# Optimization experiments

Hardware: AMD Instinct MI355X
Metric: run time of the kernel (lower is better)

Reference implementation:

```python
import jax, jax.numpy as jnp
import numpy as np

DIM = 512
K_ALL = 11
K_TOP = 4
DOMAIN = 10
EPS = 1e-12
NEG_INF = -1e30

def _normalize(x):
    n = jnp.linalg.norm(x, axis=-1, keepdims=True)
    return x / jnp.maximum(n, EPS)

def _leaky(x):
    return jax.nn.leaky_relu(x, 0.01)

def setup_inputs():
    key = jax.random.key(0)
    ks = jax.random.split(key, 16)
    Bp, Lp, Bg, Lg = 128, 256, 64, 512
    probes = jax.random.normal(ks[0], (1, Bp, Lp, DIM), jnp.float32)
    gallery = jax.random.normal(ks[1], (1, Bg, Lg, DIM), jnp.float32)
    probe_lengths = jax.random.randint(ks[2], (1, Bp), 1, Lp + 1)
    gallery_lengths = jax.random.randint(ks[3], (1, Bg), 1, Lg + 1)
    proxies_p = jax.random.normal(ks[4], (K_ALL, DIM), jnp.float32) * 0.06
    proxies_g = jax.random.normal(ks[5], (K_ALL, DIM), jnp.float32) * 0.06
    transform_W = jax.random.normal(ks[6], (DOMAIN, DIM), jnp.float32) * 0.06
    transform_b = jnp.zeros((DOMAIN,), jnp.float32)
    probe_W = jnp.eye(DIM, dtype=jnp.float32)  # nn.init.eye_
    probe_b = jnp.zeros((DIM,), jnp.float32)
    # pooler MLP weights stacked over the 11 experts; init_weights: N(0, 0.001), zero bias
    pool_W1 = jax.random.normal(ks[7], (K_ALL, 2 * DIM, 3 * DIM), jnp.float32) * 1e-3
    pool_b1 = jnp.zeros((K_ALL, 2 * DIM), jnp.float32)
    pool_W2 = jax.random.normal(ks[8], (K_ALL, 2 * DIM, 2 * DIM), jnp.float32) * 1e-3
    pool_b2 = jnp.zeros((K_ALL, 2 * DIM), jnp.float32)
    pool_W3 = jax.random.normal(ks[9], (K_ALL, DIM, 2 * DIM), jnp.float32) * 1e-3
    pool_b3 = jnp.zeros((K_ALL, DIM), jnp.float32)
    return dict(probes=probes, gallery=gallery, probe_lengths=probe_lengths,
                gallery_lengths=gallery_lengths, proxies_p=proxies_p, proxies_g=proxies_g,
                transform_W=transform_W, transform_b=transform_b, probe_W=probe_W,
                probe_b=probe_b, pool_W1=pool_W1, pool_b1=pool_b1, pool_W2=pool_W2,
                pool_b2=pool_b2, pool_W3=pool_W3, pool_b3=pool_b3)

def reference(probes, gallery, probe_lengths, gallery_lengths, proxies_p, proxies_g,
              transform_W, transform_b, probe_W, probe_b,
              pool_W1, pool_b1, pool_W2, pool_b2, pool_W3, pool_b3):
    def fuse(feat, length, proxies, use_probe_linear):
        # feat: [L, D], length: scalar int; masked equivalent of feat[:length]
        L = feat.shape[0]
        fmask = (jnp.arange(L) < length).astype(feat.dtype)[:, None]  # [L, 1]
        lp = jnp.maximum(length, 1).astype(feat.dtype)
        normed = _normalize(feat)
        tf = _normalize(feat @ transform_W.T + transform_b)        # [L, 10]
        tp = _normalize(proxies @ transform_W.T + transform_b)      # [K_ALL, 10]
        sims = tf @ tp.T                                            # [L, K_ALL]
        gsim = (sims * fmask).sum(0)                                # [K_ALL]
        _, idx = jax.lax.top_k(gsim, K_TOP)
        mean = (feat * fmask).sum(0) / lp                           # [D]
        var = (((feat - mean) ** 2) * fmask).sum(0) / lp            # biased variance
        summary = jnp.concatenate([jnp.tile(mean[None], (K_TOP, 1)),
                                   jnp.tile(var[None], (K_TOP, 1)),
                                   proxies[idx]], axis=-1)          # [K_TOP, 3D]
        # expert-gathered pooler MLPs (dropout = identity in eval)
        h = _leaky(jnp.einsum('koi,ki->ko', pool_W1[idx], summary) + pool_b1[idx])
        h = _leaky(jnp.einsum('koi,ki->ko', pool_W2[idx], h) + pool_b2[idx])
        ctx = _leaky(jnp.einsum('koi,ki->ko', pool_W3[idx], h) + pool_b3[idx])  # [K_TOP, D]
        q = feat @ probe_W.T + probe_b if use_probe_linear else feat
        scores = q @ ctx.T                                          # [L, K_TOP]
        scores = jnp.where(fmask > 0, scores, NEG_INF)
        w = jax.nn.softmax(scores, axis=0)                          # softmax over set dim
        return jnp.einsum('ld,lk->kd', normed, w)                   # [K_TOP, D]

    p, g = probes[0], gallery[0]
    pl, gl = probe_lengths[0], gallery_lengths[0]
    final_probe = jax.vmap(lambda f, l: fuse(f, l, proxies_p, True))(p, pl)
    final_gallery = jax.vmap(lambda f, l: fuse(f, l, proxies_g, False))(g, gl)
    return (final_probe,
            proxies_p @ transform_W.T + transform_b,
            final_gallery,
            proxies_g @ transform_W.T + transform_b)
```

## Files before the change

### kernel.cpp

```cpp
#include <hip/hip_runtime.h>
#include <hip/hip_bf16.h>

namespace {

using us = unsigned short;
typedef __attribute__((ext_vector_type(8))) short bf16x8;
typedef __attribute__((ext_vector_type(4))) float f32x4;
typedef __attribute__((ext_vector_type(4))) unsigned short us4;
typedef __attribute__((ext_vector_type(4))) unsigned int u32x4;

constexpr int DIM_ = 512, KALL = 11, DOM = 10, NPROBE = 128, NSETS = 192;
constexpr int LPR = 256, LGA = 512;

constexpr size_t O_OUT1 = 0;
constexpr size_t O_OUT2 = (size_t)NPROBE * 4 * DIM_;
constexpr size_t O_OUT3 = O_OUT2 + KALL * DOM;
constexpr size_t O_OUT4 = O_OUT3 + (size_t)64 * 4 * DIM_;

constexpr size_t F_TP   = 64;
constexpr size_t F_IDX  = 320;
constexpr size_t F_S0A  = 1600;
constexpr size_t F_WQ   = 4096;
constexpr size_t F_GP   = 495616;
constexpr size_t F_SUMM = 514048;
constexpr size_t F_H1   = 612352;
constexpr size_t F_PART = F_H1;
constexpr size_t F_CTXW = F_H1;
constexpr size_t F_H2   = 1693696;
constexpr size_t F_ACC  = F_H2;
constexpr size_t F_CTX  = 2775040;
constexpr size_t F_WT   = 3315712;
constexpr size_t WS_FLOATS = 3446784;
constexpr size_t WS_BYTES  = WS_FLOATS * 4;

__device__ __forceinline__ float b2f(us u) { return __uint_as_float(((unsigned)u) << 16); }
__device__ __forceinline__ us f2b(float x) {
    unsigned u = __float_as_uint(x);
    u += 0x7FFF + ((u >> 16) & 1);
    return (us)(u >> 16);
}
__device__ __forceinline__ float ldT(const float* p) { return *p; }
__device__ __forceinline__ float ldT(const us* p) { return b2f(*p); }
__device__ __forceinline__ void stT(float* p, float v) { *p = v; }
__device__ __forceinline__ void stT(us* p, float v) { *p = f2b(v); }

__device__ __forceinline__ bf16x8 loadA(const us* p) { return *(const bf16x8*)p; }
__device__ __forceinline__ bf16x8 loadA(const float* p) {
    f32x4 a = *(const f32x4*)p, b = *(const f32x4*)(p + 4);
    bf16x8 r;
#pragma unroll
    for (int j = 0; j < 4; ++j) { r[j] = (short)f2b(a[j]); r[4 + j] = (short)f2b(b[j]); }
    return r;
}

__device__ __forceinline__ void gload_lds16(const us* g, us* l) {
    __builtin_amdgcn_global_load_lds(
        (const __attribute__((address_space(1))) void*)g,
        (__attribute__((address_space(3))) void*)l, 16, 0, 0);
}

__device__ __forceinline__ void decode64(int bx, int& set, int& base, int& L) {
    if (bx < 512) { set = bx >> 2; base = (bx & 3) * 64; L = LPR; }
    else { set = NPROBE + ((bx - 512) >> 3); base = ((bx - 512) & 7) * 64; L = LGA; }
}

__global__ void detect_kernel(const unsigned int* probeW_bits, int* flag) {
    if (threadIdx.x == 0) *flag = (probeW_bits[0] == 0x3F800000u) ? 0 : 1;
}

template <typename T>
__device__ void proxies_body(const T* pp, const T* pg, const T* tW, const T* tb,
                             float* wsf, T* dout) {
    int b = blockIdx.x;
    int fam = b / KALL, i = b % KALL;
    int lane = threadIdx.x;
    const T* src = fam ? pg : pp;
    float t[DOM];
#pragma unroll
    for (int r = 0; r < DOM; ++r) t[r] = 0.f;
    for (int d = lane; d < DIM_; d += 64) {
        float x = ldT(src + (size_t)i * DIM_ + d);
#pragma unroll
        for (int r = 0; r < DOM; ++r) t[r] += x * ldT(tW + (size_t)r * DIM_ + d);
    }
#pragma unroll
    for (int off = 32; off >= 1; off >>= 1)
#pragma unroll
        for (int r = 0; r < DOM; ++r) t[r] += __shfl_xor(t[r], off, 64);
#pragma unroll
    for (int r = 0; r < DOM; ++r) t[r] += ldT(tb + r);
    float nn = 0.f;
#pragma unroll
    for (int r = 0; r < DOM; ++r) nn += t[r] * t[r];
    float inv = 1.0f / fmaxf(sqrtf(nn), 1e-12f);
    if (lane < DOM) {
        size_t base = fam ? O_OUT4 : O_OUT2;
        stT(dout + base + i * DOM + lane, t[lane]);
        wsf[F_TP + fam * 128 + i * DOM + lane] = t[lane] * inv;
    }
}
__global__ void proxies_kernel(const int* flag, const void* pp, const void* pg,
                               const void* tW, const void* tb, float* wsf, void* dout) {
    if (*flag)
        proxies_body<us>((const us*)pp, (const us*)pg, (const us*)tW, (const us*)tb, wsf, (us*)dout);
    else
        proxies_body<float>((const float*)pp, (const float*)pg, (const float*)tW, (const float*)tb, wsf, (float*)dout);
}

template <typename T>
__device__ void sums_body(const T* probes, const T* gallery, const int* plen,
                          const int* glen, float* wsf) {
    int bx = blockIdx.x, set = bx >> 2, c = bx & 3;
    bool probe = set < NPROBE;
    int L = probe ? LPR : LGA;
    const T* feat = probe ? probes + (size_t)set * L * DIM_
                          : gallery + (size_t)(set - NPROBE) * L * DIM_;
    int len = probe ? plen[set] : glen[set - NPROBE];
    int len_eff = min(max(len, 1), L);
    int r0 = (c * len_eff) >> 2, r1 = ((c + 1) * len_eff) >> 2;
    __shared__ float psum[DIM_], psq[DIM_];
    int tid = threadIdx.x, w = tid >> 6, lane = tid & 63;
    psum[tid] = 0.f; psum[tid + 256] = 0.f;
    psq[tid] = 0.f; psq[tid + 256] = 0.f;
    __syncthreads();
    float asum[8] = {0,0,0,0,0,0,0,0}, asq[8] = {0,0,0,0,0,0,0,0};
    for (int l = r0 + w * 2; l < r1; l += 8) {
        bool two = (l + 1 < r1);
        float f0[8], f1[8];
        if constexpr (sizeof(T) == 2) {
            u32x4 ra = *(const u32x4*)(feat + (size_t)l * DIM_ + lane * 8);
            u32x4 rb = two ? *(const u32x4*)(feat + (size_t)(l + 1) * DIM_ + lane * 8)
                           : (u32x4){0, 0, 0, 0};
#pragma unroll
            for (int q = 0; q < 4; ++q) {
                f0[2*q] = __uint_as_float(ra[q] << 16);
                f0[2*q+1] = __uint_as_float(ra[q] & 0xFFFF0000u);
                f1[2*q] = __uint_as_float(rb[q] << 16);
                f1[2*q+1] = __uint_as_float(rb[q] & 0xFFFF0000u);
            }
        } else {
            const T* rp = feat + (size_t)l * DIM_ + lane * 8;
            f32x4 a0 = *(const f32x4*)rp, a1 = *(const f32x4*)(rp + 4);
#pragma unroll
            for (int j = 0; j < 4; ++j) { f0[j] = a0[j]; f0[4+j] = a1[j]; }
            if (two) {
                const T* rq = feat + (size_t)(l + 1) * DIM_ + lane * 8;
                f32x4 b0 = *(const f32x4*)rq, b1 = *(const f32x4*)(rq + 4);
#pragma unroll
                for (int j = 0; j < 4; ++j) { f1[j] = b0[j]; f1[4+j] = b1[j]; }
            } else {
#pragma unroll
                for (int j = 0; j < 8; ++j) f1[j] = 0.f;
            }
        }
#pragma unroll
        for (int j = 0; j < 8; ++j) {
            asum[j] += f0[j] + f1[j];
            asq[j] += f0[j] * f0[j] + f1[j] * f1[j];
        }
    }
#pragma unroll
    for (int j = 0; j < 8; ++j) {
        atomicAdd(&psum[lane * 8 + j], asum[j]);
        atomicAdd(&psq[lane * 8 + j], asq[j]);
    }
    __syncthreads();
    float* P = wsf + F_PART + (size_t)bx * 1024;
    P[tid] = psum[tid]; P[tid + 256] = psum[tid + 256];
    P[512 + tid] = psq[tid]; P[768 + tid] = psq[tid + 256];
}
__global__ __launch_bounds__(256) void sums_kernel(const int* flag, const void* probes,
        const void* gallery, const int* plen, const int* glen, float* wsf) {
    if (*flag) sums_body<us>((const us*)probes, (const us*)gallery, plen, glen, wsf);
    else sums_body<float>((const float*)probes, (const float*)gallery, plen, glen, wsf);
}

template <typename T>
__device__ void sims_body(const T* probes, const T* gallery, const int* plen,
                          const int* glen, const T* tW, float* wsf) {
    int bx = blockIdx.x, set, base, L;
    decode64(bx, set, base, L);
    bool probe = set < NPROBE;
    int len = probe ? plen[set] : glen[set - NPROBE];
    int len_eff = min(max(len, 1), L);
    float* GP = wsf + F_GP + (size_t)bx * 12;
    int tid = threadIdx.x;
    if (base >= len_eff) { if (tid < KALL) GP[tid] = 0.f; return; }
    const T* feat = probe ? probes + (size_t)set * L * DIM_
                          : gallery + (size_t)(set - NPROBE) * L * DIM_;
    __shared__ __align__(16) float tile[4][320];
    __shared__ float tpl[KALL * DOM];
    __shared__ float gs[16];
    if (tid < KALL * DOM) tpl[tid] = wsf[F_TP + (probe ? 0 : 128) + tid];
    if (tid < 16) gs[tid] = 0.f;
    int w = tid >> 6, lane = tid & 63, lm = lane & 15, quad = lane >> 4;

    bf16x8 bq[16];
#pragma unroll
    for (int s = 0; s < 16; ++s) {
        if (lm < DOM) bq[s] = loadA(tW + (size_t)lm * DIM_ + s * 32 + quad * 8);
        else bq[s] = (bf16x8){0, 0, 0, 0, 0, 0, 0, 0};
    }
    int m0 = base + w * 16;
    const T* Ap = feat + (size_t)(m0 + lm) * DIM_ + quad * 8;
    f32x4 acc = (f32x4){0.f, 0.f, 0.f, 0.f};
    float vsq = 0.f;
#pragma unroll
    for (int s = 0; s < 16; ++s) {
        bf16x8 a;
        if constexpr (sizeof(T) == 2) {
            a = *(const bf16x8*)(Ap + s * 32);
#pragma unroll
            for (int j = 0; j < 8; ++j) { float x = b2f((us)a[j]); vsq += x * x; }
        } else {
            f32x4 p0 = *(const f32x4*)(Ap + s * 32), p1 = *(const f32x4*)(Ap + s * 32 + 4);
#pragma unroll
            for (int j = 0; j < 4; ++j) {
                vsq += p0[j] * p0[j] + p1[j] * p1[j];
                a[j] = (short)f2b(p0[j]); a[4 + j] = (short)f2b(p1[j]);
            }
        }
        acc = __builtin_amdgcn_mfma_f32_16x16x32_bf16(a, bq[s], acc, 0, 0, 0);
    }
    vsq += __shfl_xor(vsq, 16, 64);
    vsq += __shfl_xor(vsq, 32, 64);
    {
        int rown = m0 + lm;
        if (quad == 0 && rown < len_eff)
            wsf[F_WQ + (size_t)set * 2560 + (size_t)rown * 5 + 4] =
                1.0f / fmaxf(sqrtf(vsq), 1e-12f);
    }
#pragma unroll
    for (int r = 0; r < 4; ++r) tile[w][(quad * 4 + r) * 20 + lm] = acc[r];
    __syncthreads();

    float gacc[KALL];
#pragma unroll
    for (int k = 0; k < KALL; ++k) gacc[k] = 0.f;
    if (lane < 16) {
        int row = m0 + lane;
        if (row < len_eff) {
            const float* tr = &tile[w][lane * 20];
            f32x4 t0 = *(const f32x4*)tr, t1 = *(const f32x4*)(tr + 4);
            float tv[DOM] = {t0[0], t0[1], t0[2], t0[3], t1[0], t1[1], t1[2], t1[3], tr[8], tr[9]};
            float nn = 0.f;
#pragma unroll
            for (int r = 0; r < DOM; ++r) nn += tv[r] * tv[r];
            float inv = 1.0f / fmaxf(sqrtf(nn), 1e-12f);
#pragma unroll
            for (int k = 0; k < KALL; ++k) {
                float s = 0.f;
#pragma unroll
                for (int r = 0; r < DOM; ++r) s += tv[r] * tpl[k * DOM + r];
                gacc[k] = s * inv;
            }
        }
    }
#pragma unroll
    for (int off = 8; off >= 1; off >>= 1)
#pragma unroll
        for (int k = 0; k < KALL; ++k) gacc[k] += __shfl_xor(gacc[k], off, 64);
    if (lane == 0)
#pragma unroll
        for (int k = 0; k < KALL; ++k) atomicAdd(&gs[k], gacc[k]);
    __syncthreads();
    if (tid < KALL) GP[tid] = gs[tid];
}
__global__ __launch_bounds__(256, 3) void sims_kernel(const int* flag, const void* probes,
        const void* gallery, const int* plen, const int* glen, const void* tW, float* wsf) {
    if (*flag) sims_body<us>((const us*)probes, (const us*)gallery, plen, glen, (const us*)tW, wsf);
    else sims_body<float>((const float*)probes, (const float*)gallery, plen, glen, (const float*)tW, wsf);
}

__global__ void statsfin_kernel(const int* plen, const int* glen, float* wsf) {
    int set = blockIdx.x, tid = threadIdx.x;
    bool probe = set < NPROBE;
    int len = probe ? plen[set] : glen[set - NPROBE];
    float lp = (float)max(len, 1);
    const float* P = wsf + F_PART + (size_t)set * 4 * 1024;
    us* SUMM = (us*)(wsf + F_SUMM);
    for (int d = tid; d < DIM_; d += 256) {
        float s = P[d] + P[1024 + d] + P[2048 + d] + P[3072 + d];
        float q = P[512 + d] + P[1536 + d] + P[2560 + d] + P[3584 + d];
        float m = s / lp;
        float v = q / lp - m * m;
        SUMM[(size_t)set * 1024 + d] = f2b(m);
        SUMM[(size_t)set * 1024 + DIM_ + d] = f2b(v);
    }
    if (tid == 0) {
        int nch = probe ? 4 : 8;
        int gb = probe ? set * 4 : 512 + (set - NPROBE) * 8;
        float g[KALL];
        for (int i = 0; i < KALL; ++i) {
            float s = 0.f;
            for (int c = 0; c < nch; ++c) s += wsf[F_GP + (size_t)(gb + c) * 12 + i];
            g[i] = s;
        }
        int* idx4 = (int*)(wsf + F_IDX);
        for (int kk = 0; kk < 4; ++kk) {
            int bi = 0; float bv = g[0];
            for (int i = 1; i < KALL; ++i)
                if (g[i] > bv) { bv = g[i]; bi = i; }
            idx4[set * 4 + kk] = bi;
            g[bi] = -3e38f;
        }
    }
}

template <typename T>
__device__ void wt_body(const T* W, us* WT) {
    __shared__ us t[64][65];
    int bi = blockIdx.y * 64, bj = blockIdx.x * 64, tid = threadIdx.x;
    for (int i = tid; i < 4096; i += 256) {
        int r = i >> 6, cc = i & 63;
        t[r][cc] = (sizeof(T) == 2) ? ((const us*)W)[(size_t)(bi + r) * DIM_ + bj + cc]
                                    : f2b(ldT(W + (size_t)(bi + r) * DIM_ + bj + cc));
    }
    __syncthreads();
    for (int i = tid; i < 4096; i += 256) {
        int r = i >> 6, cc = i & 63;
        WT[(size_t)(bj + r) * DIM_ + bi + cc] = t[cc][r];
    }
}
__global__ void wt_kernel(const int* flag, const void* W, us* WT) {
    if (*flag) wt_body<us>((const us*)W, WT);
    else wt_body<float>((const float*)W, WT);
}

template <int M, int KTOT, int L1>
__global__ __launch_bounds__(256) void mlp_one(const int* flag, const void* Wv,
        const void* biasv, const void* ppv, const void* pgv, const us* X, us* Y) {
    constexpr int MT = M / 64;
    int flagv = *flag;
    __shared__ us SM[16384];
    us* As = SM;
    us* Bs = SM + 8192;
    int bx = blockIdx.x;
    int nt = bx / (MT * KALL);
    int rem = bx - nt * (MT * KALL);
    int e = rem % KALL;
    int mt = rem / KALL;
    int tid = threadIdx.x, w = tid >> 6, lane = tid & 63;
    int lm = lane & 15, quad = lane >> 4;
    const int RS = L1 ? 1024 : KTOT;
    int s0 = nt * 64;
    int srow = tid >> 4;
    int csrc = (tid & 15) ^ (srow & 7);
    us* lA = As + tid * 8;
    us* lB = Bs + tid * 8;
    const size_t arow = (size_t)e * M + mt * 64 + srow;
    const us*    AbB = (const us*)Wv + arow * KTOT + csrc * 8;
    const float* AbF = (const float*)Wv + arow * KTOT + csrc * 8;
    const us* Xbase = X + ((size_t)(L1 ? 0 : e * NSETS) + s0 + srow) * RS + csrc * 8;
    const us* PbB = nullptr;
    const float* PbF = nullptr;
    if (L1) {
        PbB = (const us*)(nt < 2 ? ppv : pgv) + (size_t)e * DIM_ + csrc * 8;
        PbF = (const float*)(nt < 2 ? ppv : pgv) + (size_t)e * DIM_ + csrc * 8;
    }
    f32x4 acc[4];
#pragma unroll
    for (int j = 0; j < 4; ++j) acc[j] = (f32x4){0.f, 0.f, 0.f, 0.f};
    int ar = w * 16 + lm, aswz = ar & 7;

    for (int k0 = 0; k0 < KTOT; k0 += 128) {
        __syncthreads();
        if (flagv) {
#pragma unroll
            for (int i = 0; i < 4; ++i)
                gload_lds16(AbB + (size_t)(i * 16) * KTOT + k0, lA + i * 2048);
        } else {
#pragma unroll
            for (int i = 0; i < 4; ++i)
                *(bf16x8*)(lA + i * 2048) = loadA(AbF + (size_t)(i * 16) * KTOT + k0);
        }
        if (!L1 || k0 < 1024) {
#pragma unroll
            for (int i = 0; i < 4; ++i)
                gload_lds16(Xbase + (size_t)(i * 16) * RS + k0, lB + i * 2048);
        } else if (flagv) {
#pragma unroll
            for (int i = 0; i < 4; ++i)
                gload_lds16(PbB + (k0 - 1024), lB + i * 2048);
        } else {
            bf16x8 v = loadA(PbF + (k0 - 1024));
#pragma unroll
            for (int i = 0; i < 4; ++i)
                *(bf16x8*)(lB + i * 2048) = v;
        }
        __syncthreads();
#pragma unroll
        for (int ks = 0; ks < 4; ++ks) {
            int cg = ks * 4 + quad;
            bf16x8 a = *(const bf16x8*)(As + ar * 128 + ((cg ^ aswz) * 8));
#pragma unroll
            for (int j = 0; j < 4; ++j) {
                int br = j * 16 + lm;
                bf16x8 b = *(const bf16x8*)(Bs + br * 128 + ((cg ^ (br & 7)) * 8));
                acc[j] = __builtin_amdgcn_mfma_f32_16x16x32_bf16(a, b, acc[j], 0, 0, 0);
            }
        }
    }
    int m0 = mt * 64 + w * 16 + quad * 4;
    float bv[4];
#pragma unroll
    for (int r = 0; r < 4; ++r)
        bv[r] = flagv ? b2f(((const us*)biasv)[(size_t)e * M + m0 + r])
                      : ((const float*)biasv)[(size_t)e * M + m0 + r];
#pragma unroll
    for (int j = 0; j < 4; ++j) {
        int s = s0 + j * 16 + lm;
        us4 pk;
#pragma unroll
        for (int r = 0; r < 4; ++r) {
            float v = acc[j][r] + bv[r];
            v = v > 0.f ? v : 0.01f * v;
            pk[r] = f2b(v);
        }
        *(us4*)(Y + ((size_t)e * NSETS + s) * M + m0) = pk;
    }
}

__global__ void fold_kernel(const us* CTX, const us* WT, us* CTXW) {
    int nt = blockIdx.x, mtb = blockIdx.y;
    int e = mtb >> 1, sub = mtb & 1;
    int row0 = e * NSETS + sub * 64;
    int tid = threadIdx.x, w = tid >> 6, lane = tid & 63;
    int lm = lane & 15, quad = lane >> 4, kq = quad * 8;
    const us* Ap = CTX + ((size_t)row0 + w * 16 + lm) * DIM_ + kq;
    int n0 = nt * 64;
    const us* Bp = WT + (size_t)(n0 + lm) * DIM_ + kq;
    f32x4 acc[4];
#pragma unroll
    for (int j = 0; j < 4; ++j) acc[j] = (f32x4){0.f, 0.f, 0.f, 0.f};
#pragma unroll 2
    for (int kc = 0; kc < DIM_; kc += 32) {
        bf16x8 a = *(const bf16x8*)(Ap + kc);
#pragma unroll
        for (int j = 0; j < 4; ++j) {
            bf16x8 b = *(const bf16x8*)(Bp + kc + (size_t)j * 16 * DIM_);
            acc[j] = __builtin_amdgcn_mfma_f32_16x16x32_bf16(a, b, acc[j], 0, 0, 0);
        }
    }
    int mrow = row0 + w * 16 + quad * 4;
#pragma unroll
    for (int j = 0; j < 4; ++j)
#pragma unroll
        for (int r = 0; r < 4; ++r)
            CTXW[(size_t)(mrow + r) * DIM_ + n0 + j * 16 + lm] = f2b(acc[j][r]);
}

template <typename T>
__device__ void s0a_body(const us* CTX, const T* pb, float* S0A) {
    int tid = threadIdx.x, w = tid >> 6, lane = tid & 63;
    int row = blockIdx.x * 4 + w;
    bf16x8 cv = *(const bf16x8*)(CTX + (size_t)row * DIM_ + lane * 8);
    float s = 0.f;
#pragma unroll
    for (int j = 0; j < 8; ++j) s += b2f((us)cv[j]) * ldT(pb + lane * 8 + j);
#pragma unroll
    for (int off = 32; off >= 1; off >>= 1) s += __shfl_xor(s, off, 64);
    if (lane == 0) S0A[row] = s;
}
__global__ void s0a_kernel(const int* flag, const us* CTX, const void* pb, float* S0A) {
    if (*flag) s0a_body<us>(CTX, (const us*)pb, S0A);
    else s0a_body<float>(CTX, (const float*)pb, S0A);
}

template <typename T>
__device__ void score_body(const T* probes, const T* gallery, const int* plen,
                           const int* glen, float* wsf) {
    int bx = blockIdx.x, set, base, L;
    decode64(bx, set, base, L);
    bool probe = set < NPROBE;
    int len = probe ? plen[set] : glen[set - NPROBE];
    int len_eff = min(max(len, 1), L);
    if (base >= len_eff) return;
    const T* feat = probe ? probes + (size_t)set * L * DIM_
                          : gallery + (size_t)(set - NPROBE) * L * DIM_;
    int tid = threadIdx.x, w = tid >> 6, lane = tid & 63;
    int lm = lane & 15, quad = lane >> 4;
    const int* idx4 = (const int*)(wsf + F_IDX);
    const us* CTXW = (const us*)(wsf + F_CTXW);
    const us* CTXR = (const us*)(wsf + F_CTX);
    bf16x8 bq[16];
    float s0v = 0.f;
    if (lm < 4) {
        int row = idx4[set * 4 + lm] * NSETS + set;
        const us* src = (probe ? CTXW : CTXR) + (size_t)row * DIM_ + quad * 8;
#pragma unroll
        for (int s = 0; s < 16; ++s) bq[s] = *(const bf16x8*)(src + s * 32);
        s0v = probe ? wsf[F_S0A + row] : 0.f;
    } else {
#pragma unroll
        for (int s = 0; s < 16; ++s) bq[s] = (bf16x8){0, 0, 0, 0, 0, 0, 0, 0};
    }
    int m0 = base + w * 16;
    const T* Ap = feat + (size_t)(m0 + lm) * DIM_ + quad * 8;
    f32x4 acc = (f32x4){0.f, 0.f, 0.f, 0.f};
#pragma unroll
    for (int s = 0; s < 16; ++s) {
        bf16x8 a = loadA(Ap + s * 32);
        acc = __builtin_amdgcn_mfma_f32_16x16x32_bf16(a, bq[s], acc, 0, 0, 0);
    }
    if (lm < 4) {
        float* wq = wsf + F_WQ + (size_t)set * 2560;
#pragma unroll
        for (int r = 0; r < 4; ++r) {
            int row = m0 + quad * 4 + r;
            wq[(size_t)row * 5 + lm] = acc[r] + s0v;
        }
    }
}
__global__ __launch_bounds__(256, 3) void score_kernel(const int* flag, const void* probes,
        const void* gallery, const int* plen, const int* glen, float* wsf) {
    if (*flag) score_body<us>((const us*)probes, (const us*)gallery, plen, glen, wsf);
    else score_body<float>((const float*)probes, (const float*)gallery, plen, glen, wsf);
}

__global__ void softmax_kernel(const int* plen, const int* glen, float* wsf) {
    int set = blockIdx.x, tid = threadIdx.x, k = tid >> 6, lane = tid & 63;
    bool probe = set < NPROBE;
    int L = probe ? LPR : LGA;
    int len = probe ? plen[set] : glen[set - NPROBE];
    int len_eff = min(max(len, 1), L);
    float* wq = wsf + F_WQ + (size_t)set * 2560;
    float cv[8];
    int n = 0;
    float m = -3e38f;
    for (int l = lane; l < len_eff; l += 64) {
        cv[n] = wq[(size_t)l * 5 + k];
        m = fmaxf(m, cv[n]);
        ++n;
    }
#pragma unroll
    for (int off = 32; off >= 1; off >>= 1) m = fmaxf(m, __shfl_xor(m, off, 64));
    float se = 0.f;
    for (int i = 0; i < n; ++i) se += __expf(cv[i] - m);
#pragma unroll
    for (int off = 32; off >= 1; off >>= 1) se += __shfl_xor(se, off, 64);
    float invs = 1.0f / se;
    n = 0;
    for (int l = lane; l < len_eff; l += 64) {
        wq[(size_t)l * 5 + k] = __expf(cv[n] - m) * invs * wq[(size_t)l * 5 + 4];
        ++n;
    }
}

template <typename T>
__device__ void accum_body(const T* probes, const T* gallery, const int* plen,
                           const int* glen, float* wsf) {
    int bx = blockIdx.x, set = bx >> 2, c = bx & 3;
    bool probe = set < NPROBE;
    int L = probe ? LPR : LGA;
    const T* feat = probe ? probes + (size_t)set * L * DIM_
                          : gallery + (size_t)(set - NPROBE) * L * DIM_;
    int len = probe ? plen[set] : glen[set - NPROBE];
    int len_eff = min(max(len, 1), L);
    int r0 = (c * len_eff) >> 2, r1 = ((c + 1) * len_eff) >> 2;
    int tid = threadIdx.x, g = tid >> 8, t = tid & 255;
    __shared__ float cf[512];
    __shared__ float pbuf[2048];
    int nr = r1 - r0;
    const float* wq = wsf + F_WQ + (size_t)set * 2560;
    for (int p = tid; p < nr * 4; p += 512)
        cf[p] = wq[(size_t)(r0 + (p >> 2)) * 5 + (p & 3)];
    __syncthreads();
    float ac[8] = {0.f, 0.f, 0.f, 0.f, 0.f, 0.f, 0.f, 0.f};
#pragma unroll 4
    for (int l = r0 + g; l < r1; l += 2) {
        float f0, f1;
        if constexpr (sizeof(T) == 2) {
            unsigned u = *(const unsigned*)((const us*)feat + (size_t)l * DIM_ + t * 2);
            f0 = __uint_as_float(u << 16);
            f1 = __uint_as_float(u & 0xFFFF0000u);
        } else {
            const T* rp = feat + (size_t)l * DIM_ + t * 2;
            f0 = rp[0]; f1 = rp[1];
        }
        f32x4 cc = *(const f32x4*)&cf[(l - r0) * 4];
#pragma unroll
        for (int k = 0; k < 4; ++k) {
            ac[k * 2] += f0 * cc[k];
            ac[k * 2 + 1] += f1 * cc[k];
        }
    }
    if (g == 1) {
#pragma unroll
        for (int i = 0; i < 8; ++i) pbuf[i * 256 + t] = ac[i];
    }
    __syncthreads();
    if (g == 0) {
        float* P = wsf + F_ACC + (size_t)bx * 2048;
#pragma unroll
        for (int k = 0; k < 4; ++k) {
            P[k * 512 + t * 2] = ac[k * 2] + pbuf[(k * 2) * 256 + t];
            P[k * 512 + t * 2 + 1] = ac[k * 2 + 1] + pbuf[(k * 2 + 1) * 256 + t];
        }
    }
}
__global__ __launch_bounds__(512) void accum_kernel(const int* flag, const void* probes,
        const void* gallery, const int* plen, const int* glen, float* wsf) {
    if (*flag) accum_body<us>((const us*)probes, (const us*)gallery, plen, glen, wsf);
    else accum_body<float>((const float*)probes, (const float*)gallery, plen, glen, wsf);
}

template <typename T>
__device__ void reduce_body(const float* wsf, T* dout) {
    int set = blockIdx.x, d = threadIdx.x;
    const float* A = wsf + F_ACC + (size_t)set * 4 * 2048;
    size_t ob = (set < NPROBE) ? O_OUT1 + (size_t)set * 2048
                               : O_OUT3 + (size_t)(set - NPROBE) * 2048;
#pragma unroll
    for (int k = 0; k < 4; ++k) {
        float s = A[k * 512 + d] + A[2048 + k * 512 + d] + A[4096 + k * 512 + d] + A[6144 + k * 512 + d];
        stT(dout + ob + k * 512 + d, s);
    }
}
__global__ __launch_bounds__(512) void reduce_kernel(const int* flag, const float* wsf, void* dout) {
    if (*flag) reduce_body<us>(wsf, (us*)dout);
    else reduce_body<float>(wsf, (float*)dout);
}

}

extern "C" void kernel_launch(void* const* d_in, const int* in_sizes, int n_in,
                              void* d_out, int out_size, void* d_ws, size_t ws_size,
                              hipStream_t stream) {
    if (ws_size < WS_BYTES) return;
    float* wsf = (float*)d_ws;
    int* flag = (int*)d_ws;
    us* SUMM = (us*)(wsf + F_SUMM);
    us* H1 = (us*)(wsf + F_H1);
    us* H2 = (us*)(wsf + F_H2);
    us* CTXb = (us*)(wsf + F_CTX);
    us* CTXW = (us*)(wsf + F_CTXW);
    us* WT = (us*)(wsf + F_WT);
    const int* plen = (const int*)d_in[2];
    const int* glen = (const int*)d_in[3];

    detect_kernel<<<1, 64, 0, stream>>>((const unsigned int*)d_in[8], flag);
    proxies_kernel<<<22, 64, 0, stream>>>(flag, d_in[4], d_in[5], d_in[6], d_in[7], wsf, d_out);
    wt_kernel<<<dim3(8, 8), 256, 0, stream>>>(flag, d_in[8], WT);
    sums_kernel<<<NSETS * 4, 256, 0, stream>>>(flag, d_in[0], d_in[1], plen, glen, wsf);
    sims_kernel<<<1024, 256, 0, stream>>>(flag, d_in[0], d_in[1], plen, glen, d_in[6], wsf);
    statsfin_kernel<<<NSETS, 256, 0, stream>>>(plen, glen, wsf);

    mlp_one<1024, 1536, 1><<<3 * 16 * KALL, 256, 0, stream>>>(
        flag, d_in[10], d_in[11], d_in[4], d_in[5], SUMM, H1);
    mlp_one<1024, 1024, 0><<<3 * 16 * KALL, 256, 0, stream>>>(
        flag, d_in[12], d_in[13], d_in[4], d_in[5], H1, H2);
    mlp_one<512, 1024, 0><<<3 * 8 * KALL, 256, 0, stream>>>(
        flag, d_in[14], d_in[15], d_in[4], d_in[5], H2, CTXb);

    fold_kernel<<<dim3(8, 22), 256, 0, stream>>>(CTXb, WT, CTXW);
    s0a_kernel<<<528, 256, 0, stream>>>(flag, CTXb, d_in[9], wsf + F_S0A);
    score_kernel<<<1024, 256, 0, stream>>>(flag, d_in[0], d_in[1], plen, glen, wsf);
    softmax_kernel<<<NSETS, 256, 0, stream>>>(plen, glen, wsf);
    accum_kernel<<<NSETS * 4, 512, 0, stream>>>(flag, d_in[0], d_in[1], plen, glen, wsf);
    reduce_kernel<<<NSETS, 512, 0, stream>>>(flag, wsf, d_out);
}
```

Baseline: 415.6 us.

## Fold proxy term of first MLP layer into bias and double-buffer MLP GEMM

The constant proxy slice of the first pooler layer (the last 512 input columns) is now precomputed once per expert as an effective bias for the probe side and the gallery side, in a new small kernel. This shrinks the layer-1 GEMM reduction from 1536 to 1024. The MLP GEMM kernel is also restructured: weight fragments are loaded straight into registers instead of through LDS, and activation tiles use a double-buffered LDS pipeline with 64-wide K steps, so loads overlap compute. The cost is one extra launch and a fixed 16-step K loop, which assumes every layer's K is 1024.

Result: slower. 429.5 us (+3.4%).

```diff
diff --git a/kernel.cpp b/kernel.cpp
--- a/kernel.cpp
+++ b/kernel.cpp
@@ -30,7 +30,8 @@
 constexpr size_t F_ACC  = F_H2;
 constexpr size_t F_CTX  = 2775040;
 constexpr size_t F_WT   = 3315712;
-constexpr size_t WS_FLOATS = 3446784;
+constexpr size_t F_BEFF = 3446784;
+constexpr size_t WS_FLOATS = F_BEFF + 2 * KALL * 1024;
 constexpr size_t WS_BYTES  = WS_FLOATS * 4;
 
 __device__ __forceinline__ float b2f(us u) { return __uint_as_float(((unsigned)u) << 16); }
@@ -47,6 +48,12 @@
 __device__ __forceinline__ bf16x8 loadA(const us* p) { return *(const bf16x8*)p; }
 __device__ __forceinline__ bf16x8 loadA(const float* p) {
     f32x4 a = *(const f32x4*)p, b = *(const f32x4*)(p + 4);
+    bf16x8 r;
+#pragma unroll
+    for (int j = 0; j < 4; ++j) { r[j] = (short)f2b(a[j]); r[4 + j] = (short)f2b(b[j]); }
+    return r;
+}
+__device__ __forceinline__ bf16x8 pack8(f32x4 a, f32x4 b) {
     bf16x8 r;
 #pragma unroll
     for (int j = 0; j < 4; ++j) { r[j] = (short)f2b(a[j]); r[4 + j] = (short)f2b(b[j]); }
@@ -105,6 +112,55 @@
         proxies_body<us>((const us*)pp, (const us*)pg, (const us*)tW, (const us*)tb, wsf, (us*)dout);
     else
         proxies_body<float>((const float*)pp, (const float*)pg, (const float*)tW, (const float*)tb, wsf, (float*)dout);
+}
+
+template <typename T>
+__device__ void pbias_body(const T* W1, const T* b1, const T* pp, const T* pg, float* beff) {
+    int bx = blockIdx.x;
+    int e = bx >> 4, ch = bx & 15;
+    int tid = threadIdx.x;
+    int om = tid >> 2, sub = tid & 3;
+    int m = ch * 64 + om;
+    const T* wr = W1 + ((size_t)e * 1024 + m) * 1536 + 1024 + sub * 128;
+    const T* pr = pp + (size_t)e * DIM_ + sub * 128;
+    const T* gr = pg + (size_t)e * DIM_ + sub * 128;
+    float sp = 0.f, sg = 0.f;
+    if constexpr (sizeof(T) == 2) {
+#pragma unroll 4
+        for (int k = 0; k < 128; k += 2) {
+            unsigned wv = *(const unsigned*)(wr + k);
+            unsigned pv = *(const unsigned*)(pr + k);
+            unsigned gv = *(const unsigned*)(gr + k);
+            float w0 = __uint_as_float(wv << 16), w1 = __uint_as_float(wv & 0xFFFF0000u);
+            float p0 = __uint_as_float(pv << 16), p1 = __uint_as_float(pv & 0xFFFF0000u);
+            float g0 = __uint_as_float(gv << 16), g1 = __uint_as_float(gv & 0xFFFF0000u);
+            sp += w0 * p0 + w1 * p1;
+            sg += w0 * g0 + w1 * g1;
+        }
+    } else {
+#pragma unroll 2
+        for (int k = 0; k < 128; k += 4) {
+            f32x4 wv = *(const f32x4*)(wr + k);
+            f32x4 pv = *(const f32x4*)(pr + k);
+            f32x4 gv = *(const f32x4*)(gr + k);
+#pragma unroll
+            for (int q = 0; q < 4; ++q) { sp += wv[q] * pv[q]; sg += wv[q] * gv[q]; }
+        }
+    }
+    sp += __shfl_xor(sp, 1, 64); sp += __shfl_xor(sp, 2, 64);
+    sg += __shfl_xor(sg, 1, 64); sg += __shfl_xor(sg, 2, 64);
+    if (sub == 0) {
+        float bb = ldT(b1 + (size_t)e * 1024 + m);
+        beff[(size_t)e * 1024 + m] = bb + sp;
+        beff[(size_t)(KALL + e) * 1024 + m] = bb + sg;
+    }
+}
+__global__ void pbias_kernel(const int* flag, const void* W1, const void* b1,
+                             const void* pp, const void* pg, float* beff) {
+    if (*flag)
+        pbias_body<us>((const us*)W1, (const us*)b1, (const us*)pp, (const us*)pg, beff);
+    else
+        pbias_body<float>((const float*)W1, (const float*)b1, (const float*)pp, (const float*)pg, beff);
 }
 
 template <typename T>
@@ -327,14 +383,13 @@
     else wt_body<float>((const float*)W, WT);
 }
 
-template <int M, int KTOT, int L1>
+template <int M, int KS, int L1>
 __global__ __launch_bounds__(256) void mlp_one(const int* flag, const void* Wv,
-        const void* biasv, const void* ppv, const void* pgv, const us* X, us* Y) {
+        const void* biasv, const us* X, us* Y, const float* beff) {
     constexpr int MT = M / 64;
+    constexpr int NK = 16;
     int flagv = *flag;
-    __shared__ us SM[16384];
-    us* As = SM;
-    us* Bs = SM + 8192;
+    __shared__ us SM[8192];
     int bx = blockIdx.x;
     int nt = bx / (MT * KALL);
     int rem = bx - nt * (MT * KALL);
@@ -342,71 +397,91 @@
     int mt = rem / KALL;
     int tid = threadIdx.x, w = tid >> 6, lane = tid & 63;
     int lm = lane & 15, quad = lane >> 4;
-    const int RS = L1 ? 1024 : KTOT;
     int s0 = nt * 64;
-    int srow = tid >> 4;
-    int csrc = (tid & 15) ^ (srow & 7);
-    us* lA = As + tid * 8;
-    us* lB = Bs + tid * 8;
-    const size_t arow = (size_t)e * M + mt * 64 + srow;
-    const us*    AbB = (const us*)Wv + arow * KTOT + csrc * 8;
-    const float* AbF = (const float*)Wv + arow * KTOT + csrc * 8;
-    const us* Xbase = X + ((size_t)(L1 ? 0 : e * NSETS) + s0 + srow) * RS + csrc * 8;
-    const us* PbB = nullptr;
-    const float* PbF = nullptr;
-    if (L1) {
-        PbB = (const us*)(nt < 2 ? ppv : pgv) + (size_t)e * DIM_ + csrc * 8;
-        PbF = (const float*)(nt < 2 ? ppv : pgv) + (size_t)e * DIM_ + csrc * 8;
-    }
+    const size_t aoff = ((size_t)e * M + mt * 64 + w * 16 + lm) * KS + quad * 8;
+    const float* AF = (const float*)Wv + aoff;
+    const us*    AB = (const us*)Wv + aoff;
+    int xrow0 = (L1 ? 0 : e * NSETS) + s0;
+    int slot0 = w * 64 + lane, slot1 = slot0 + 256;
+    int brow0 = slot0 >> 3, bcol0 = (slot0 & 7) ^ (brow0 & 7);
+    int brow1 = slot1 >> 3, bcol1 = (slot1 & 7) ^ (brow1 & 7);
+    const us* Xs0 = X + ((size_t)(xrow0 + brow0)) * 1024 + bcol0 * 8;
+    const us* Xs1 = X + ((size_t)(xrow0 + brow1)) * 1024 + bcol1 * 8;
+    us* ls0 = SM + slot0 * 8;
+    us* ls1 = SM + slot1 * 8;
+
     f32x4 acc[4];
 #pragma unroll
     for (int j = 0; j < 4; ++j) acc[j] = (f32x4){0.f, 0.f, 0.f, 0.f};
-    int ar = w * 16 + lm, aswz = ar & 7;
-
-    for (int k0 = 0; k0 < KTOT; k0 += 128) {
-        __syncthreads();
+
+    bf16x8 a0[2], a1[2];
+    f32x4 pan[4];
+
+    auto issueB = [&](int par, int k0) {
+        gload_lds16(Xs0 + k0, ls0 + par * 4096);
+        gload_lds16(Xs1 + k0, ls1 + par * 4096);
+    };
+    auto loadAx = [&](int k0, bf16x8* adst) {
         if (flagv) {
-#pragma unroll
-            for (int i = 0; i < 4; ++i)
-                gload_lds16(AbB + (size_t)(i * 16) * KTOT + k0, lA + i * 2048);
+            adst[0] = *(const bf16x8*)(AB + k0);
+            adst[1] = *(const bf16x8*)(AB + k0 + 32);
         } else {
-#pragma unroll
-            for (int i = 0; i < 4; ++i)
-                *(bf16x8*)(lA + i * 2048) = loadA(AbF + (size_t)(i * 16) * KTOT + k0);
-        }
-        if (!L1 || k0 < 1024) {
-#pragma unroll
-            for (int i = 0; i < 4; ++i)
-                gload_lds16(Xbase + (size_t)(i * 16) * RS + k0, lB + i * 2048);
-        } else if (flagv) {
-#pragma unroll
-            for (int i = 0; i < 4; ++i)
-                gload_lds16(PbB + (k0 - 1024), lB + i * 2048);
-        } else {
-            bf16x8 v = loadA(PbF + (k0 - 1024));
-#pragma unroll
-            for (int i = 0; i < 4; ++i)
-                *(bf16x8*)(lB + i * 2048) = v;
-        }
-        __syncthreads();
-#pragma unroll
-        for (int ks = 0; ks < 4; ++ks) {
-            int cg = ks * 4 + quad;
-            bf16x8 a = *(const bf16x8*)(As + ar * 128 + ((cg ^ aswz) * 8));
+            pan[0] = *(const f32x4*)(AF + k0);
+            pan[1] = *(const f32x4*)(AF + k0 + 4);
+            pan[2] = *(const f32x4*)(AF + k0 + 32);
+            pan[3] = *(const f32x4*)(AF + k0 + 36);
+        }
+    };
+    auto packA = [&](bf16x8* adst) {
+        if (!flagv) {
+            adst[0] = pack8(pan[0], pan[1]);
+            adst[1] = pack8(pan[2], pan[3]);
+        }
+    };
+    auto compute = [&](int par, const bf16x8* a) {
+        const us* Bb = SM + par * 4096;
+#pragma unroll
+        for (int ks = 0; ks < 2; ++ks)
 #pragma unroll
             for (int j = 0; j < 4; ++j) {
                 int br = j * 16 + lm;
-                bf16x8 b = *(const bf16x8*)(Bs + br * 128 + ((cg ^ (br & 7)) * 8));
-                acc[j] = __builtin_amdgcn_mfma_f32_16x16x32_bf16(a, b, acc[j], 0, 0, 0);
+                int cg = ks * 4 + quad;
+                bf16x8 b = *(const bf16x8*)(Bb + br * 64 + ((cg ^ (br & 7)) * 8));
+                acc[j] = __builtin_amdgcn_mfma_f32_16x16x32_bf16(a[ks], b, acc[j], 0, 0, 0);
             }
-        }
-    }
+    };
+
+    issueB(0, 0);
+    loadAx(0, a0);
+    packA(a0);
+    __syncthreads();
+#pragma unroll 1
+    for (int t = 0; t < NK; t += 2) {
+        int k1 = (t + 1) * 64, k2 = (t + 2) * 64;
+        if (t + 1 < NK) { issueB(1, k1); loadAx(k1, a1); }
+        compute(0, a0);
+        if (t + 1 < NK) packA(a1);
+        __syncthreads();
+        if (t + 1 < NK) {
+            if (t + 2 < NK) { issueB(0, k2); loadAx(k2, a0); }
+            compute(1, a1);
+            if (t + 2 < NK) packA(a0);
+            __syncthreads();
+        }
+    }
+
     int m0 = mt * 64 + w * 16 + quad * 4;
     float bv[4];
-#pragma unroll
-    for (int r = 0; r < 4; ++r)
-        bv[r] = flagv ? b2f(((const us*)biasv)[(size_t)e * M + m0 + r])
-                      : ((const float*)biasv)[(size_t)e * M + m0 + r];
+    if (L1) {
+        const float* be = beff + ((size_t)((nt < 2) ? 0 : KALL) + e) * 1024 + m0;
+#pragma unroll
+        for (int r = 0; r < 4; ++r) bv[r] = be[r];
+    } else {
+#pragma unroll
+        for (int r = 0; r < 4; ++r)
+            bv[r] = flagv ? b2f(((const us*)biasv)[(size_t)e * M + m0 + r])
+                          : ((const float*)biasv)[(size_t)e * M + m0 + r];
+    }
 #pragma unroll
     for (int j = 0; j < 4; ++j) {
         int s = s0 + j * 16 + lm;
@@ -641,17 +716,18 @@
 
     detect_kernel<<<1, 64, 0, stream>>>((const unsigned int*)d_in[8], flag);
     proxies_kernel<<<22, 64, 0, stream>>>(flag, d_in[4], d_in[5], d_in[6], d_in[7], wsf, d_out);
+    pbias_kernel<<<176, 256, 0, stream>>>(flag, d_in[10], d_in[11], d_in[4], d_in[5], wsf + F_BEFF);
     wt_kernel<<<dim3(8, 8), 256, 0, stream>>>(flag, d_in[8], WT);
     sums_kernel<<<NSETS * 4, 256, 0, stream>>>(flag, d_in[0], d_in[1], plen, glen, wsf);
     sims_kernel<<<1024, 256, 0, stream>>>(flag, d_in[0], d_in[1], plen, glen, d_in[6], wsf);
     statsfin_kernel<<<NSETS, 256, 0, stream>>>(plen, glen, wsf);
 
     mlp_one<1024, 1536, 1><<<3 * 16 * KALL, 256, 0, stream>>>(
-        flag, d_in[10], d_in[11], d_in[4], d_in[5], SUMM, H1);
+        flag, d_in[10], nullptr, SUMM, H1, wsf + F_BEFF);
     mlp_one<1024, 1024, 0><<<3 * 16 * KALL, 256, 0, stream>>>(
-        flag, d_in[12], d_in[13], d_in[4], d_in[5], H1, H2);
+        flag, d_in[12], d_in[13], H1, H2, nullptr);
     mlp_one<512, 1024, 0><<<3 * 8 * KALL, 256, 0, stream>>>(
-        flag, d_in[14], d_in[15], d_in[4], d_in[5], H2, CTXb);
+        flag, d_in[14], d_in[15], H2, CTXb, nullptr);
 
     fold_kernel<<<dim3(8, 22), 256, 0, stream>>>(CTXb, WT, CTXW);
     s0a_kernel<<<528, 256, 0, stream>>>(flag, CTXb, d_in[9], wsf + F_S0A);
```
